# Optimization experiments

Hardware: AMD Instinct MI355X
Metric: run time of the kernel (lower is better)

## Reference

```python
import jax, jax.numpy as jnp
import numpy as np

B, T, C = 2, 1024, 1024
H = 16
HD = C // H
S = 512   # short_term_memory_size
L = 1024  # sum(long_term_memory_size)
THETA = 10000.0


def setup_inputs() -> dict:
    key = jax.random.key(0)
    ks = jax.random.split(key, 7)
    return {
        "x": jax.random.normal(ks[0], (B, T, C), jnp.float32),
        "short_term_memory": jax.random.normal(ks[1], (B, S, C), jnp.float32),
        "long_q": jax.random.normal(ks[2], (B, L, H, HD), jnp.float32),
        "long_k": jax.random.normal(ks[3], (B, L, H, HD), jnp.float32),
        "long_v": jax.random.normal(ks[4], (B, L, H, HD), jnp.float32),
        "w_attn": jax.random.normal(ks[5], (C, 3 * C), jnp.float32) * 0.02,
        "w_proj": jax.random.normal(ks[6], (C, C), jnp.float32) * 0.02,
    }


def _rope_cos_sin(seq_len, dim, theta):
    # llama-style precompute_freqs_cis: freqs over even indices, angles = t * freq
    inv = 1.0 / (theta ** (jnp.arange(0, dim, 2, dtype=jnp.float32) / dim))
    t = jnp.arange(seq_len, dtype=jnp.float32)
    ang = jnp.outer(t, inv)  # [seq, dim//2]
    return jnp.cos(ang), jnp.sin(ang)


def _apply_rope(x, cos, sin):
    # x: [B, seq, H, hd] viewed as interleaved complex pairs (llama apply_rotary_emb)
    xr = x.reshape(*x.shape[:-1], HD // 2, 2)
    x0, x1 = xr[..., 0], xr[..., 1]
    c = cos[None, :, None, :]
    s = sin[None, :, None, :]
    o0 = x0 * c - x1 * s
    o1 = x0 * s + x1 * c
    return jnp.stack([o0, o1], axis=-1).reshape(x.shape)


def _memory_mask():
    # create_memory_mask: tril over M=L+S+T, rows [L, L+S) fully visible
    M = L + S + T
    m = np.tril(np.ones((M, M), dtype=np.float32))
    m[L:L + S, :] = 1.0
    return jnp.asarray(m)


_MASK = _memory_mask()


def reference(x, short_term_memory, long_q, long_k, long_v, w_attn, w_proj):
    # prepend short-term memory tokens, project qkv
    xcat = jnp.concatenate([short_term_memory, x], axis=1)          # [B, S+T, C]
    qkv = xcat @ w_attn                                             # [B, S+T, 3C]
    q, k, v = jnp.split(qkv, 3, axis=-1)
    q = q.reshape(B, S + T, H, HD)
    k = k.reshape(B, S + T, H, HD)
    v = v.reshape(B, S + T, H, HD)
    # in-place rotary on the last S+T positions (long-term part untouched)
    cos, sin = _rope_cos_sin(S + T, HD, THETA)
    q = _apply_rope(q, cos, sin)
    k = _apply_rope(k, cos, sin)
    # concat pre-rotated long-term memory in front
    q = jnp.concatenate([long_q, q], axis=1)                        # [B, M, H, hd]
    k = jnp.concatenate([long_k, k], axis=1)
    v = jnp.concatenate([long_v, v], axis=1)
    q, k, v = (t.transpose(0, 2, 1, 3) for t in (q, k, v))          # [B, H, M, hd]
    att = jnp.einsum('bhqd,bhkd->bhqk', q, k) * (1.0 / jnp.sqrt(jnp.float32(HD)))
    att = jnp.where(_MASK == 0, -jnp.inf, att)
    att = jax.nn.softmax(att, axis=-1)
    y = jnp.einsum('bhqk,bhkd->bhqd', att, v)                       # [B, H, M, hd]
    y = y.transpose(0, 2, 1, 3).reshape(B, L + S + T, C)
    y = y[:, -T:, :] @ w_proj                                       # [B, T, C]
    return y
```

## Files before the change

kernel.cpp:

```cpp
#include <hip/hip_runtime.h>
#include <math.h>

#define BB 2
#define TT 1024
#define CC 1024
#define HH 16
#define HD 64
#define SS 512
#define LL 1024
#define ST 1536
#define MM 2560
#define C3 3072

typedef __attribute__((ext_vector_type(8))) short short8;
typedef __attribute__((ext_vector_type(4))) short short4v;
typedef __attribute__((ext_vector_type(4))) float floatx4;

__device__ __forceinline__ unsigned short f2bf(float f) {
    union { float f; unsigned u; } v; v.f = f;
    unsigned r = v.u + 0x7fffu + ((v.u >> 16) & 1u);
    return (unsigned short)(r >> 16);
}
__device__ __forceinline__ float bf2f(short s) {
    union { unsigned u; float f; } v;
    v.u = ((unsigned)(unsigned short)s) << 16;
    return v.f;
}

__device__ __forceinline__ void gl_lds16(const short* g, short* l) {
    __builtin_amdgcn_global_load_lds(
        (const __attribute__((address_space(1))) void*)g,
        (__attribute__((address_space(3))) void*)l,
        16, 0, 0);
}

__global__ __launch_bounds__(256)
void prep_all(const float* __restrict__ x, const float* __restrict__ stm,
              const float* __restrict__ w_attn, const float* __restrict__ w_proj,
              const float* __restrict__ lk, const float* __restrict__ lv,
              short* __restrict__ Xb, short* __restrict__ WaT,
              short* __restrict__ WpT, short* __restrict__ Kg,
              short* __restrict__ Vt, float* __restrict__ tab)
{
    __shared__ __align__(16) char smem[9216];
    const int blk = blockIdx.x;
    const int t = threadIdx.x;

    if (blk < 3072) {
        const int idx = blk * 256 + t;
        const int rg  = idx >> 8;
        const int c   = (idx & 255) << 2;
        const int b   = rg >= ST;
        const int r   = rg - b * ST;
        const float* src = (r < SS) ? (stm + ((size_t)b * SS + r) * CC + c)
                                    : (x   + ((size_t)b * TT + (r - SS)) * CC + c);
        float4 v = *(const float4*)src;
        short4v o;
        o.x = (short)f2bf(v.x); o.y = (short)f2bf(v.y);
        o.z = (short)f2bf(v.z); o.w = (short)f2bf(v.w);
        *(short4v*)(Xb + (size_t)rg * CC + c) = o;
    } else if (blk < 7168) {
        const bool isA = blk < 6144;
        const int bx = isA ? (blk - 3072) : (blk - 6144);
        const int nblk = isA ? 96 : 32;
        const int Nd = isA ? C3 : CC;
        const float* W = isA ? w_attn : w_proj;
        short* WT = isA ? WaT : WpT;
        const int n0 = (bx % nblk) * 32, k0 = (bx / nblk) * 32;
        float (*Tl)[33] = (float(*)[33])smem;
        const int r = t >> 3, c4 = (t & 7) << 2;
        float4 v = *(const float4*)(W + (size_t)(k0 + r) * Nd + n0 + c4);
        Tl[r][c4 + 0] = v.x; Tl[r][c4 + 1] = v.y;
        Tl[r][c4 + 2] = v.z; Tl[r][c4 + 3] = v.w;
        __syncthreads();
        short4v o;
        o.x = (short)f2bf(Tl[c4 + 0][r]); o.y = (short)f2bf(Tl[c4 + 1][r]);
        o.z = (short)f2bf(Tl[c4 + 2][r]); o.w = (short)f2bf(Tl[c4 + 3][r]);
        *(short4v*)(WT + (size_t)(n0 + r) * CC + k0 + c4) = o;
    } else if (blk < 7360) {
        const int idx = (blk - 7168) * 256 + t;
        const int r = idx >> 5, e = idx & 31;
        const float inv = powf(10000.0f, -(float)e * (1.0f / 32.0f));
        float sn, cs;
        sincosf((float)r * inv, &sn, &cs);
        tab[idx * 2] = cs;
        tab[idx * 2 + 1] = sn;
    } else {
        const int bx = blk - 7360;
        const int bh = bx >> 4, j0 = (bx & 15) * 64;
        const int b = bh >> 4, h = bh & 15;
        short (*Tl)[72] = (short(*)[72])smem;
        const int jr = t >> 2, c16 = (t & 3) << 4;
        const size_t si = (((size_t)b * LL + j0 + jr) * HH + h) * HD + c16;
        short kk[16], vv[16];
        #pragma unroll
        for (int u = 0; u < 4; u++) {
            float4 kv = *(const float4*)(lk + si + 4 * u);
            float4 vf = *(const float4*)(lv + si + 4 * u);
            kk[4*u+0] = (short)f2bf(kv.x); kk[4*u+1] = (short)f2bf(kv.y);
            kk[4*u+2] = (short)f2bf(kv.z); kk[4*u+3] = (short)f2bf(kv.w);
            vv[4*u+0] = (short)f2bf(vf.x); vv[4*u+1] = (short)f2bf(vf.y);
            vv[4*u+2] = (short)f2bf(vf.z); vv[4*u+3] = (short)f2bf(vf.w);
        }
        short* kdst = Kg + ((size_t)bh * MM + j0 + jr) * HD + c16;
        *(short8*)kdst       = *(short8*)&kk[0];
        *(short8*)(kdst + 8) = *(short8*)&kk[8];
        #pragma unroll
        for (int u = 0; u < 16; u++) Tl[jr][c16 + u] = vv[u];
        __syncthreads();
        const int r = t >> 2, c = t & 3;
        short o0[8], o1[8];
        #pragma unroll
        for (int u = 0; u < 8; u++) {
            o0[u] = Tl[c * 16 + u][r];
            o1[u] = Tl[c * 16 + 8 + u][r];
        }
        short* vdst = Vt + ((size_t)bh * HD + r) * MM + j0 + c * 16;
        *(short8*)vdst       = *(short8*)&o0[0];
        *(short8*)(vdst + 8) = *(short8*)&o1[0];
    }
}

__global__ __launch_bounds__(256)
void qkv_gemm(const short* __restrict__ A, const short* __restrict__ Bt,
              const float* __restrict__ RT,
              short* __restrict__ Qo, short* __restrict__ Ko, short* __restrict__ Vo)
{
    __shared__ short As[128 * 64];
    __shared__ short Bs[128 * 64];
    __shared__ short Et[128 * 132];
    const int b = blockIdx.z;
    const int row0 = blockIdx.y * 128, col0 = blockIdx.x * 128;
    const int tid = threadIdx.x;
    const int w = tid >> 6, l = tid & 63, quad = l >> 4, cl = l & 15;
    const int wr = w >> 1, wc = w & 1;

    const int reg  = col0 >> 10;
    const bool hasQ = (row0 >= SS);
    if (reg == 0 && !hasQ) return;

    const int srow8 = l >> 3;
    const int sl8   = l & 7;
    const int chA0  = (sl8 - (srow8 >> 1)) & 7;
    const int chA1  = (sl8 - 4 - (srow8 >> 1)) & 7;
    const short* gA = A + ((size_t)b * ST + row0 + w * 32 + srow8) * CC;
    const short* gB = Bt + ((size_t)(col0 + w * 32 + srow8)) * CC;
    short* lA = &As[(w * 32) * 64 + l * 8];
    short* lB = &Bs[(w * 32) * 64 + l * 8];

    floatx4 acc[4][4];
    #pragma unroll
    for (int mi = 0; mi < 4; mi++)
        #pragma unroll
        for (int ni = 0; ni < 4; ni++) acc[mi][ni] = (floatx4){0.f, 0.f, 0.f, 0.f};

    for (int k0 = 0; k0 < CC; k0 += 64) {
        __syncthreads();
        gl_lds16(gA + k0 + chA0 * 8,                     lA);
        gl_lds16(gA + (size_t)8  * CC + k0 + chA1 * 8,   lA + 512);
        gl_lds16(gA + (size_t)16 * CC + k0 + chA0 * 8,   lA + 1024);
        gl_lds16(gA + (size_t)24 * CC + k0 + chA1 * 8,   lA + 1536);
        gl_lds16(gB + k0 + chA0 * 8,                     lB);
        gl_lds16(gB + (size_t)8  * CC + k0 + chA1 * 8,   lB + 512);
        gl_lds16(gB + (size_t)16 * CC + k0 + chA0 * 8,   lB + 1024);
        gl_lds16(gB + (size_t)24 * CC + k0 + chA1 * 8,   lB + 1536);
        __syncthreads();
        #pragma unroll
        for (int ks = 0; ks < 2; ks++) {
            const int slot = (ks * 4 + quad + (cl >> 1)) & 7;
            short8 af[4], bf[4];
            #pragma unroll
            for (int mi = 0; mi < 4; mi++)
                af[mi] = *(const short8*)&As[(wr * 64 + mi * 16 + cl) * 64 + slot * 8];
            #pragma unroll
            for (int ni = 0; ni < 4; ni++)
                bf[ni] = *(const short8*)&Bs[(wc * 64 + ni * 16 + cl) * 64 + slot * 8];
            #pragma unroll
            for (int mi = 0; mi < 4; mi++)
                #pragma unroll
                for (int ni = 0; ni < 4; ni++)
                    acc[mi][ni] = __builtin_amdgcn_mfma_f32_16x16x32_bf16(
                        af[mi], bf[ni], acc[mi][ni], 0, 0, 0);
        }
    }

    #pragma unroll
    for (int ni = 0; ni < 4; ni++) {
        const int c_local = wc * 64 + ni * 16 + cl;
        const int e = (c_local & 63) >> 1;
        #pragma unroll
        for (int mi = 0; mi < 4; mi++) {
            #pragma unroll
            for (int r = 0; r < 4; r++) {
                const int R_local = wr * 64 + mi * 16 + quad * 4 + r;
                const int R = row0 + R_local;
                float v = acc[mi][ni][r];
                if (reg < 2) {
                    const float2 tt = ((const float2*)RT)[R * 32 + e];
                    float po = __shfl_xor(v, 1);
                    float out = ((cl & 1) == 0) ? (v * tt.x - po * tt.y)
                                                : (po * tt.y + v * tt.x);
                    unsigned short bfv = f2bf(out);
                    int ob = __shfl_xor((int)bfv, 1);
                    if ((cl & 1) == 0) {
                        unsigned word = (unsigned)bfv | (((unsigned)ob & 0xffffu) << 16);
                        *(unsigned*)&Et[R_local * 132 + c_local] = word;
                    }
                } else {
                    Et[c_local * 132 + R_local] = (short)f2bf(v);
                }
            }
        }
    }
    __syncthreads();

    const int hh0 = (col0 & 1023) >> 6;
    if (reg < 2) {
        #pragma unroll
        for (int hf = 0; hf < 2; hf++) {
            const int hh = hh0 + hf;
            short* dstb = (reg == 0)
                ? Qo + (((size_t)b * HH + hh) * TT + (row0 - SS)) * HD
                : Ko + (((size_t)b * HH + hh) * MM + LL + row0) * HD;
            #pragma unroll
            for (int it = 0; it < 4; it++) {
                const int idx = it * 2048 + tid * 8;
                const int r = idx >> 6, d = idx & 63;
                short4v v0 = *(const short4v*)&Et[r * 132 + hf * 64 + d];
                short4v v1 = *(const short4v*)&Et[r * 132 + hf * 64 + d + 4];
                short8 vv;
                #pragma unroll
                for (int u = 0; u < 4; u++) { vv[u] = v0[u]; vv[u + 4] = v1[u]; }
                *(short8*)(dstb + idx) = vv;
            }
        }
    } else {
        #pragma unroll
        for (int it = 0; it < 8; it++) {
            const int idx = it * 2048 + tid * 8;
            const int c = idx >> 7, r0 = idx & 127;
            const int hh = hh0 + (c >> 6), d = c & 63;
            short4v v0 = *(const short4v*)&Et[c * 132 + r0];
            short4v v1 = *(const short4v*)&Et[c * 132 + r0 + 4];
            short8 vv;
            #pragma unroll
            for (int u = 0; u < 4; u++) { vv[u] = v0[u]; vv[u + 4] = v1[u]; }
            *(short8*)(Vo + (((size_t)b * HH + hh) * HD + d) * MM + LL + row0 + r0) = vv;
        }
    }
}

#define PSP 72
#define PSW (32 * PSP)
#define VS_OFF 4096
#define PS_OFF 8192
__global__ __launch_bounds__(256, 4)
void attn_mfma(const short* __restrict__ Qg, const short* __restrict__ Kg,
               const short* __restrict__ Vt, short* __restrict__ Op,
               float* __restrict__ Lp)
{
    __shared__ __align__(16) short L[17408];

    const int bh = blockIdx.x;
    const int q0 = (7 - blockIdx.y) * 128;
    const int piece = blockIdx.z;
    const int tid = threadIdx.x, w = tid >> 6, l = tid & 63;
    const int quad = l >> 4, cl = l & 15;

    short8 qa[2][2];
    #pragma unroll
    for (int g = 0; g < 2; g++) {
        const short* qptr = Qg + ((size_t)bh * TT + q0 + w * 32 + g * 16 + cl) * HD + quad * 8;
        qa[g][0] = *(const short8*)qptr;
        qa[g][1] = *(const short8*)(qptr + 32);
    }

    floatx4 o[2][4];
    float rs[2][4];
    #pragma unroll
    for (int g = 0; g < 2; g++)
        #pragma unroll
        for (int r = 0; r < 4; r++) {
            rs[g][r] = 0.f;
            o[g][r] = (floatx4){0.f, 0.f, 0.f, 0.f};
        }

    const int srow_lo = l >> 3;
    const int sslot  = l & 7;
    const int ch0 = (sslot - (srow_lo >> 1)) & 7;
    const int ch1 = (sslot - (4 + (srow_lo >> 1))) & 7;
    const int rowi0 = w * 16 + srow_lo;
    const int rowi1 = w * 16 + 8 + srow_lo;
    const short* kgb = Kg + (size_t)bh * MM * HD;
    const short* vbase = Vt + (size_t)bh * HD * MM;
    short* ldsK0 = &L[(w * 16) * 64];
    short* ldsK1 = &L[(w * 16 + 8) * 64];
    short* ldsV0 = &L[VS_OFF + (w * 16) * 64];
    short* ldsV1 = &L[VS_OFF + (w * 16 + 8) * 64];

    const int fsA = (quad + (cl >> 1)) & 7;
    const int fsB = (quad + 4 + (cl >> 1)) & 7;
    const int psA = (quad + 2 * cl) & 7;
    const int psB = (quad + 4 + 2 * cl) & 7;

    const int ntiles = (LL + SS + q0) / 64 + 2;
    const int t_begin = piece * ntiles / 4;
    const int t_end   = (piece + 1) * ntiles / 4;

    for (int t = t_begin; t < t_end; t++) {
        const int j0 = t * 64;
        __syncthreads();
        gl_lds16(kgb + (size_t)(j0 + rowi0) * HD + ch0 * 8, ldsK0);
        gl_lds16(kgb + (size_t)(j0 + rowi1) * HD + ch1 * 8, ldsK1);
        gl_lds16(vbase + (size_t)rowi0 * MM + j0 + ch0 * 8, ldsV0);
        gl_lds16(vbase + (size_t)rowi1 * MM + j0 + ch1 * 8, ldsV1);
        __syncthreads();

        floatx4 s[2][4];
        #pragma unroll
        for (int ks = 0; ks < 4; ks++) {
            const int krow = ks * 16 + cl;
            short8 kf0 = *(const short8*)&L[krow * 64 + fsA * 8];
            short8 kf1 = *(const short8*)&L[krow * 64 + fsB * 8];
            #pragma unroll
            for (int g = 0; g < 2; g++) {
                floatx4 z = (floatx4){0.f, 0.f, 0.f, 0.f};
                z = __builtin_amdgcn_mfma_f32_16x16x32_bf16(qa[g][0], kf0, z, 0, 0, 0);
                z = __builtin_amdgcn_mfma_f32_16x16x32_bf16(qa[g][1], kf1, z, 0, 0, 0);
                s[g][ks] = z;
            }
        }

        const bool tailzone = (t >= ntiles - 2);
        #pragma unroll
        for (int g = 0; g < 2; g++) {
            const int qgb = LL + SS + q0 + w * 32 + g * 16;
            #pragma unroll
            for (int ks = 0; ks < 4; ks++) {
                #pragma unroll
                for (int r = 0; r < 4; r++) {
                    float sv = s[g][ks][r] * 0.125f;
                    if (tailzone && (j0 + ks * 16 + cl > qgb + quad * 4 + r))
                        sv = -INFINITY;
                    const float p = __expf(sv);
                    rs[g][r] += p;
                    const int qrw = quad * 4 + r;
                    const int slot = (ks * 2 + (cl >> 3) + 2 * qrw) & 7;
                    L[PS_OFF + w * PSW + (g * 16 + qrw) * PSP + slot * 8 + (cl & 7)] =
                        (short)f2bf(p);
                }
            }
        }

        __builtin_amdgcn_s_waitcnt(0xc07f);
        __builtin_amdgcn_wave_barrier();

        short8 pf[2][2];
        #pragma unroll
        for (int g = 0; g < 2; g++) {
            pf[g][0] = *(const short8*)&L[PS_OFF + w * PSW + (g * 16 + cl) * PSP + psA * 8];
            pf[g][1] = *(const short8*)&L[PS_OFF + w * PSW + (g * 16 + cl) * PSP + psB * 8];
        }
        #pragma unroll
        for (int nt = 0; nt < 4; nt++) {
            const int drow = nt * 16 + cl;
            short8 vf0 = *(const short8*)&L[VS_OFF + drow * 64 + fsA * 8];
            short8 vf1 = *(const short8*)&L[VS_OFF + drow * 64 + fsB * 8];
            #pragma unroll
            for (int g = 0; g < 2; g++) {
                o[g][nt] = __builtin_amdgcn_mfma_f32_16x16x32_bf16(pf[g][0], vf0, o[g][nt], 0, 0, 0);
                o[g][nt] = __builtin_amdgcn_mfma_f32_16x16x32_bf16(pf[g][1], vf1, o[g][nt], 0, 0, 0);
            }
        }
    }

    #pragma unroll
    for (int g = 0; g < 2; g++)
        #pragma unroll
        for (int r = 0; r < 4; r++) {
            float t2 = rs[g][r];
            t2 += __shfl_xor(t2, 1);
            t2 += __shfl_xor(t2, 2);
            t2 += __shfl_xor(t2, 4);
            t2 += __shfl_xor(t2, 8);
            if (cl == 0)
                Lp[piece * 32768 + bh * 1024 + q0 + w * 32 + g * 16 + quad * 4 + r] = t2;
        }

    __syncthreads();
    #pragma unroll
    for (int g = 0; g < 2; g++)
        #pragma unroll
        for (int r = 0; r < 4; r++) {
            const int ql = w * 32 + g * 16 + quad * 4 + r;
            #pragma unroll
            for (int nt = 0; nt < 4; nt++)
                L[ql * 68 + nt * 16 + cl] = (short)f2bf(o[g][nt][r]);
        }
    __syncthreads();
    short* ob = Op + ((size_t)(piece * 32 + bh) * 1024 + q0) * 64;
    #pragma unroll
    for (int it = 0; it < 4; it++) {
        const int idx = it * 2048 + tid * 8;
        const int q = idx >> 6, d = idx & 63;
        short4v v0 = *(const short4v*)&L[q * 68 + d];
        short4v v1 = *(const short4v*)&L[q * 68 + d + 4];
        short8 vv;
        #pragma unroll
        for (int u = 0; u < 4; u++) { vv[u] = v0[u]; vv[u + 4] = v1[u]; }
        *(short8*)(ob + idx) = vv;
    }
}

__global__ __launch_bounds__(256)
void attn_combine(const short* __restrict__ Op, const float* __restrict__ Lp,
                  short* __restrict__ Yatt)
{
    const int idx = blockIdx.x * 256 + threadIdx.x;
    const int row = idx >> 3;
    const int seg = (idx & 7) << 3;
    const float lsum = Lp[row] + Lp[32768 + row] + Lp[65536 + row] + Lp[98304 + row];
    const float inv = 1.0f / lsum;
    float acc[8] = {0.f, 0.f, 0.f, 0.f, 0.f, 0.f, 0.f, 0.f};
    #pragma unroll
    for (int p = 0; p < 4; p++) {
        short8 v = *(const short8*)(Op + ((size_t)(p * 32768) + row) * 64 + seg);
        #pragma unroll
        for (int u = 0; u < 8; u++) acc[u] += bf2f(v[u]);
    }
    short8 o8;
    #pragma unroll
    for (int u = 0; u < 8; u++) o8[u] = (short)f2bf(acc[u] * inv);
    const int bh = row >> 10, q = row & 1023;
    const int b = bh >> 4, h = bh & 15;
    *(short8*)(Yatt + ((size_t)b * TT + q) * CC + h * 64 + seg) = o8;
}

__global__ __launch_bounds__(256)
void proj_gemm(const short* __restrict__ A, const short* __restrict__ Bt,
               float* __restrict__ Co)
{
    __shared__ short As[64 * 32];
    __shared__ short Bs[64 * 32];
    const int row0 = blockIdx.y * 64, col0 = blockIdx.x * 64;
    const int tid = threadIdx.x;
    const int w = tid >> 6, l = tid & 63, quad = l >> 4, cl = l & 15;
    const int wr = w >> 1, wc = w & 1;

    const int srow = tid >> 2;
    const int schunk = ((tid & 3) - ((srow & 15) >> 1)) & 3;
    const short* gA = A + (size_t)(row0 + srow) * CC + schunk * 8;
    const short* gB = Bt + (size_t)(col0 + srow) * CC + schunk * 8;
    short* lA = &As[tid * 8];
    short* lB = &Bs[tid * 8];

    const int fs = (quad + (cl >> 1)) & 3;

    floatx4 acc[2][2];
    #pragma unroll
    for (int mi = 0; mi < 2; mi++)
        #pragma unroll
        for (int ni = 0; ni < 2; ni++) acc[mi][ni] = (floatx4){0.f, 0.f, 0.f, 0.f};

    for (int k0 = 0; k0 < CC; k0 += 32) {
        __syncthreads();
        gl_lds16(gA + k0, lA);
        gl_lds16(gB + k0, lB);
        __syncthreads();
        short8 af[2], bf[2];
        #pragma unroll
        for (int mi = 0; mi < 2; mi++)
            af[mi] = *(const short8*)&As[(wr * 32 + mi * 16 + cl) * 32 + fs * 8];
        #pragma unroll
        for (int ni = 0; ni < 2; ni++)
            bf[ni] = *(const short8*)&Bs[(wc * 32 + ni * 16 + cl) * 32 + fs * 8];
        #pragma unroll
        for (int mi = 0; mi < 2; mi++)
            #pragma unroll
            for (int ni = 0; ni < 2; ni++)
                acc[mi][ni] = __builtin_amdgcn_mfma_f32_16x16x32_bf16(
                    af[mi], bf[ni], acc[mi][ni], 0, 0, 0);
    }
    #pragma unroll
    for (int mi = 0; mi < 2; mi++)
        #pragma unroll
        for (int ni = 0; ni < 2; ni++)
            #pragma unroll
            for (int r = 0; r < 4; r++)
                Co[(size_t)(row0 + wr * 32 + mi * 16 + quad * 4 + r) * CC
                   + col0 + wc * 32 + ni * 16 + cl] = acc[mi][ni][r];
}

extern "C" void kernel_launch(void* const* d_in, const int* in_sizes, int n_in,
                              void* d_out, int out_size, void* d_ws, size_t ws_size,
                              hipStream_t stream)
{
    (void)in_sizes; (void)n_in; (void)out_size; (void)ws_size;
    const float* x      = (const float*)d_in[0];
    const float* stm    = (const float*)d_in[1];
    const float* long_k = (const float*)d_in[3];
    const float* long_v = (const float*)d_in[4];
    const float* w_attn = (const float*)d_in[5];
    const float* w_proj = (const float*)d_in[6];
    float* out = (float*)d_out;

    short* Xb   = (short*)d_ws;
    short* WaT  = Xb   + (size_t)3145728;
    short* WpT  = WaT  + (size_t)3145728;
    short* Qb   = WpT  + (size_t)1048576;
    short* Kb   = Qb   + (size_t)2097152;
    short* Vtr  = Kb   + (size_t)5242880;
    short* Yb   = Vtr  + (size_t)5242880;
    float* RTab = (float*)(Yb + (size_t)2097152);
    short* Opart = (short*)(RTab + 98304);
    float* Lpart = (float*)(Opart + (size_t)8388608);

    prep_all<<<7872, 256, 0, stream>>>(x, stm, w_attn, w_proj, long_k, long_v,
                                       Xb, WaT, WpT, Kb, Vtr, RTab);

    qkv_gemm<<<dim3(24, 12, 2), 256, 0, stream>>>(Xb, WaT, RTab, Qb, Kb, Vtr);

    attn_mfma<<<dim3(32, 8, 4), 256, 0, stream>>>(Qb, Kb, Vtr, Opart, Lpart);
    attn_combine<<<1024, 256, 0, stream>>>(Opart, Lpart, Yb);

    proj_gemm<<<dim3(16, 32), 256, 0, stream>>>(Yb, WpT, out);
}
```

Measured before the change: 197.5 us.

## Deepen proj GEMM K-tile to 64 and use DPP swaps in RoPE epilogue

The projection GEMM now stages a 64-wide K slice per iteration instead of 32, using a new swizzled LDS layout and two MFMA sub-steps per tile. This halves the number of barrier pairs and load rounds in the K loop, at the cost of doubling the LDS footprint. Separately, the RoPE epilogue of the QKV GEMM replaces __shfl_xor with DPP quad-permute moves and packs the bf16 pair with v_cvt_pk_bf16_f32. This removes LDS-based shuffles and the manual rounding code.

```diff
diff --git a/kernel.cpp b/kernel.cpp
--- a/kernel.cpp
+++ b/kernel.cpp
@@ -197,13 +197,17 @@
                 float v = acc[mi][ni][r];
                 if (reg < 2) {
                     const float2 tt = ((const float2*)RT)[R * 32 + e];
-                    float po = __shfl_xor(v, 1);
+                    union { float f; int i; } vu; vu.f = v;
+                    const float po = __int_as_float(
+                        __builtin_amdgcn_mov_dpp(vu.i, 0xB1, 0xf, 0xf, true));
                     float out = ((cl & 1) == 0) ? (v * tt.x - po * tt.y)
                                                 : (po * tt.y + v * tt.x);
-                    unsigned short bfv = f2bf(out);
-                    int ob = __shfl_xor((int)bfv, 1);
+                    union { float f; int i; } ou; ou.f = out;
+                    const int oo = __builtin_amdgcn_mov_dpp(ou.i, 0xB1, 0xf, 0xf, true);
                     if ((cl & 1) == 0) {
-                        unsigned word = (unsigned)bfv | (((unsigned)ob & 0xffffu) << 16);
+                        unsigned word;
+                        asm("v_cvt_pk_bf16_f32 %0, %1, %2"
+                            : "=v"(word) : "v"(out), "v"(__int_as_float(oo)));
                         *(unsigned*)&Et[R_local * 132 + c_local] = word;
                     }
                 } else {
@@ -440,21 +444,23 @@
 void proj_gemm(const short* __restrict__ A, const short* __restrict__ Bt,
                float* __restrict__ Co)
 {
-    __shared__ short As[64 * 32];
-    __shared__ short Bs[64 * 32];
+    __shared__ short As[64 * 64];
+    __shared__ short Bs[64 * 64];
     const int row0 = blockIdx.y * 64, col0 = blockIdx.x * 64;
     const int tid = threadIdx.x;
     const int w = tid >> 6, l = tid & 63, quad = l >> 4, cl = l & 15;
     const int wr = w >> 1, wc = w & 1;
 
-    const int srow = tid >> 2;
-    const int schunk = ((tid & 3) - ((srow & 15) >> 1)) & 3;
-    const short* gA = A + (size_t)(row0 + srow) * CC + schunk * 8;
-    const short* gB = Bt + (size_t)(col0 + srow) * CC + schunk * 8;
-    short* lA = &As[tid * 8];
-    short* lB = &Bs[tid * 8];
-
-    const int fs = (quad + (cl >> 1)) & 3;
+    const int srow_lo = l >> 3;
+    const int sslot   = l & 7;
+    const int ch0 = (sslot - (srow_lo >> 1)) & 7;
+    const int ch1 = (sslot - 4 - (srow_lo >> 1)) & 7;
+    const short* gA = A + (size_t)(row0 + w * 16 + srow_lo) * CC;
+    const short* gB = Bt + (size_t)(col0 + w * 16 + srow_lo) * CC;
+    short* lA0 = &As[(w * 16) * 64 + l * 8];
+    short* lA1 = &As[(w * 16 + 8) * 64 + l * 8];
+    short* lB0 = &Bs[(w * 16) * 64 + l * 8];
+    short* lB1 = &Bs[(w * 16 + 8) * 64 + l * 8];
 
     floatx4 acc[2][2];
     #pragma unroll
@@ -462,24 +468,30 @@
         #pragma unroll
         for (int ni = 0; ni < 2; ni++) acc[mi][ni] = (floatx4){0.f, 0.f, 0.f, 0.f};
 
-    for (int k0 = 0; k0 < CC; k0 += 32) {
-        __syncthreads();
-        gl_lds16(gA + k0, lA);
-        gl_lds16(gB + k0, lB);
-        __syncthreads();
-        short8 af[2], bf[2];
-        #pragma unroll
-        for (int mi = 0; mi < 2; mi++)
-            af[mi] = *(const short8*)&As[(wr * 32 + mi * 16 + cl) * 32 + fs * 8];
-        #pragma unroll
-        for (int ni = 0; ni < 2; ni++)
-            bf[ni] = *(const short8*)&Bs[(wc * 32 + ni * 16 + cl) * 32 + fs * 8];
-        #pragma unroll
-        for (int mi = 0; mi < 2; mi++)
+    for (int k0 = 0; k0 < CC; k0 += 64) {
+        __syncthreads();
+        gl_lds16(gA + k0 + ch0 * 8,                   lA0);
+        gl_lds16(gA + (size_t)8 * CC + k0 + ch1 * 8,  lA1);
+        gl_lds16(gB + k0 + ch0 * 8,                   lB0);
+        gl_lds16(gB + (size_t)8 * CC + k0 + ch1 * 8,  lB1);
+        __syncthreads();
+        #pragma unroll
+        for (int ks = 0; ks < 2; ks++) {
+            const int slot = (ks * 4 + quad + (cl >> 1)) & 7;
+            short8 af[2], bf[2];
+            #pragma unroll
+            for (int mi = 0; mi < 2; mi++)
+                af[mi] = *(const short8*)&As[(wr * 32 + mi * 16 + cl) * 64 + slot * 8];
             #pragma unroll
             for (int ni = 0; ni < 2; ni++)
-                acc[mi][ni] = __builtin_amdgcn_mfma_f32_16x16x32_bf16(
-                    af[mi], bf[ni], acc[mi][ni], 0, 0, 0);
+                bf[ni] = *(const short8*)&Bs[(wc * 32 + ni * 16 + cl) * 64 + slot * 8];
+            #pragma unroll
+            for (int mi = 0; mi < 2; mi++)
+                #pragma unroll
+                for (int ni = 0; ni < 2; ni++)
+                    acc[mi][ni] = __builtin_amdgcn_mfma_f32_16x16x32_bf16(
+                        af[mi], bf[ni], acc[mi][ni], 0, 0, 0);
+        }
     }
     #pragma unroll
     for (int mi = 0; mi < 2; mi++)
```

Result: no change. 199.6 us (+1.0%).
